# Kernel tuning notes

Measured on AMD Instinct MI355X. Metric: run time of the kernel, lower is better.

## Reference

```python
import jax, jax.numpy as jnp
from jax import lax
import numpy as np

B, C, H, W = 4, 256, 64, 64
CQK = C // 8  # 32


def conv3x3(x, w, b):
    # x: [B,C_in,H,W], w: [C_out,C_in,3,3], b: [C_out]
    y = lax.conv_general_dilated(x, w, window_strides=(1, 1), padding='SAME',
                                 dimension_numbers=('NCHW', 'OIHW', 'NCHW'))
    return y + b[None, :, None, None]


def setup_inputs() -> dict:
    key = jax.random.key(0)
    ks = jax.random.split(key, 8)
    scale = 0.02
    return {
        'x': jax.random.normal(ks[0], (B, C, H, W), dtype=jnp.float32),
        'wq': jax.random.normal(ks[1], (CQK, C, 3, 3), dtype=jnp.float32) * scale,
        'bq': jax.random.normal(ks[2], (CQK,), dtype=jnp.float32) * scale,
        'wk': jax.random.normal(ks[3], (CQK, C, 3, 3), dtype=jnp.float32) * scale,
        'bk': jax.random.normal(ks[4], (CQK,), dtype=jnp.float32) * scale,
        'wv': jax.random.normal(ks[5], (C, C, 3, 3), dtype=jnp.float32) * scale,
        'bv': jax.random.normal(ks[6], (C,), dtype=jnp.float32) * scale,
        'gamma': jax.random.normal(ks[7], (1,), dtype=jnp.float32) * scale,
    }


def reference(x, wq, bq, wk, bk, wv, bv, gamma):
    b, c, h, w = x.shape
    n = h * w
    # Q: [B, N, C//8]  (permute(0,2,1) of the flattened conv output)
    q = conv3x3(x, wq, bq).reshape(b, -1, n).transpose(0, 2, 1)
    # K: [B, C//8, N]
    k = conv3x3(x, wk, bk).reshape(b, -1, n)
    # s: [B, N_q, N_k]
    s = jnp.einsum('bqd,bdk->bqk', q, k)
    # NOTE: original uses Softmax(dim=-2), i.e. over the QUERY axis
    attn_T = jax.nn.softmax(s, axis=-2)
    # V: [B, C, N]
    v = conv3x3(x, wv, bv).reshape(b, c, n)
    # o = bmm(V, attn_T): [B, C, N]
    o = jnp.einsum('bcq,bqk->bck', v, attn_T).reshape(b, c, h, w)
    return x + gamma * o
```

## Files before the change

kernel.cpp:

```cpp
#include <hip/hip_runtime.h>
#include <cstddef>

#define N_PIX 4096
#define HW 64
#define LOG2E 1.4426950408889634f
#define SHIFT2 28.8539008177793f

typedef __attribute__((ext_vector_type(8))) short bf16x8;
typedef __attribute__((ext_vector_type(4))) float f32x4;

static __device__ __forceinline__ unsigned short f2bf(float f) {
    union { float f; unsigned u; } v; v.f = f;
    unsigned r = v.u + 0x7fffu + ((v.u >> 16) & 1u);
    return (unsigned short)(r >> 16);
}
static __device__ __forceinline__ float bf2f(unsigned short s) {
    union { unsigned u; float f; } v; v.u = (unsigned)s << 16;
    return v.f;
}
static __device__ __forceinline__ unsigned pack_bf16_trunc(float lo, float hi) {
    union { float f; unsigned u; } a, b; a.f = hi; b.f = lo;
    return __builtin_amdgcn_perm(a.u, b.u, 0x07060302u);
}

__global__ __launch_bounds__(256) void x_transpose(
    const float* __restrict__ x, unsigned short* __restrict__ xbf)
{
    __shared__ unsigned short Ts[64][72];
    const int tid = threadIdx.x;
    const int px0 = blockIdx.x * 64, ci0 = blockIdx.y * 64, b = blockIdx.z;
    const float* xb = x + ((size_t)b * 256 + ci0) * N_PIX;

#pragma unroll
    for (int r = 0; r < 4; ++r) {
        int c = r * 16 + (tid >> 4);
        int p4 = (tid & 15) * 4;
        float4 v = *(const float4*)&xb[(size_t)c * N_PIX + px0 + p4];
        Ts[c][p4 + 0] = f2bf(v.x);
        Ts[c][p4 + 1] = f2bf(v.y);
        Ts[c][p4 + 2] = f2bf(v.z);
        Ts[c][p4 + 3] = f2bf(v.w);
    }
    __syncthreads();
#pragma unroll
    for (int r = 0; r < 2; ++r) {
        int id = tid * 2 + r;
        int p = id >> 3, c8 = (id & 7) * 8;
        ushort4 lo, hi;
        lo.x = Ts[c8 + 0][p]; lo.y = Ts[c8 + 1][p];
        lo.z = Ts[c8 + 2][p]; lo.w = Ts[c8 + 3][p];
        hi.x = Ts[c8 + 4][p]; hi.y = Ts[c8 + 5][p];
        hi.z = Ts[c8 + 6][p]; hi.w = Ts[c8 + 7][p];
        size_t off = ((size_t)b * N_PIX + px0 + p) * 256 + ci0 + c8;
        *(ushort4*)&xbf[off]     = lo;
        *(ushort4*)&xbf[off + 4] = hi;
    }
}

__global__ __launch_bounds__(256) void w_transform(
    const float* __restrict__ wq, const float* __restrict__ wk,
    const float* __restrict__ wv, unsigned short* __restrict__ wAll)
{
    int gid = blockIdx.x * 256 + threadIdx.x;
    if (gid >= 72 * 320 * 4) return;
    int part = gid & 3;
    int m = (gid >> 2) % 320;
    int kb = gid / 1280;
    int t = kb >> 3;
    int ci0 = (kb & 7) * 32 + part * 8;
    const float* src; int co; float sc = 1.f;
    if (m < 256)      { src = wv; co = m; }
    else if (m < 288) { src = wq; co = m - 256; sc = LOG2E; }
    else              { src = wk; co = m - 288; }
    ushort4 lo, hi;
    lo.x = f2bf(sc * src[((size_t)co * 256 + ci0 + 0) * 9 + t]);
    lo.y = f2bf(sc * src[((size_t)co * 256 + ci0 + 1) * 9 + t]);
    lo.z = f2bf(sc * src[((size_t)co * 256 + ci0 + 2) * 9 + t]);
    lo.w = f2bf(sc * src[((size_t)co * 256 + ci0 + 3) * 9 + t]);
    hi.x = f2bf(sc * src[((size_t)co * 256 + ci0 + 4) * 9 + t]);
    hi.y = f2bf(sc * src[((size_t)co * 256 + ci0 + 5) * 9 + t]);
    hi.z = f2bf(sc * src[((size_t)co * 256 + ci0 + 6) * 9 + t]);
    hi.w = f2bf(sc * src[((size_t)co * 256 + ci0 + 7) * 9 + t]);
    size_t off = ((size_t)kb * 320 + m) * 32 + part * 8;
    *(ushort4*)&wAll[off]     = lo;
    *(ushort4*)&wAll[off + 4] = hi;
}

__global__ __launch_bounds__(256, 3) void conv_gemm_v3(
    const unsigned short* __restrict__ xbf, const unsigned short* __restrict__ wAll,
    const float* __restrict__ bq, const float* __restrict__ bk,
    const float* __restrict__ bv,
    unsigned short* __restrict__ vbf, unsigned short* __restrict__ qt,
    unsigned short* __restrict__ kt)
{
    const int tid = threadIdx.x;
    const int w = tid >> 6, lane = tid & 63, quad = lane >> 4, l15 = lane & 15;
    const int bx  = blockIdx.x;
    const int px0 = bx * 64;
    const int mt  = blockIdx.y;
    const int b   = blockIdx.z;
    const bool qk = (mt == 2);
    const int row0 = qk ? 256 : mt * 128;
    const int NCB  = qk ? 2 : 4;
    const int wc0  = (w & 1) * (qk ? 32 : 64);
    const int wp0  = (w >> 1) * 32;

    __shared__ unsigned short Bl[2][64 * 64];

    const unsigned short* xb = xbf + (size_t)b * N_PIX * 256;

    const int brow = tid >> 2;
    const int bp0  = (tid & 3) * 2;

    f32x4 acc[4][2];
#pragma unroll
    for (int cb = 0; cb < 4; ++cb)
#pragma unroll
        for (int jb = 0; jb < 2; ++jb) acc[cb][jb] = (f32x4){0.f, 0.f, 0.f, 0.f};

    const unsigned short* aBase = wAll + ((size_t)(row0 + wc0 + l15) * 32 + quad * 8);

    auto load_a = [&](int n, bf16x8 (&af)[2][4]) {
        const unsigned short* p = aBase + (size_t)(2 * n) * (320 * 32);
#pragma unroll
        for (int kl = 0; kl < 2; ++kl)
#pragma unroll
            for (int cb = 0; cb < 4; ++cb)
                if (cb < NCB) af[kl][cb] = *(const bf16x8*)&p[kl * (320 * 32) + cb * 512];
    };

    bf16x8 bS[2];
    auto load_b = [&](int n) {
        int t  = n >> 2;
        int ty = t / 3;
        int dy = ty - 1, dx = t - ty * 3 - 1;
        int gy = bx + dy, gx = brow + dx;
        int cio = (n & 3) * 64 + (tid & 3) * 16;
        if ((unsigned)gy < 64u && (unsigned)gx < 64u) {
            const unsigned short* s = xb + ((size_t)(gy * 64 + gx) * 256 + cio);
            bS[0] = *(const bf16x8*)&s[0];
            bS[1] = *(const bf16x8*)&s[8];
        } else {
            bS[0] = (bf16x8){0,0,0,0,0,0,0,0};
            bS[1] = (bf16x8){0,0,0,0,0,0,0,0};
        }
    };
    auto store_b = [&](int buf) {
        int p0 = (bp0 + brow) & 7;
        int p1 = (bp0 + 1 + brow) & 7;
        *(bf16x8*)&Bl[buf][brow * 64 + p0 * 8] = bS[0];
        *(bf16x8*)&Bl[buf][brow * 64 + p1 * 8] = bS[1];
    };

    auto step = [&](int n, bf16x8 (&cur)[2][4], bf16x8 (&nxt)[2][4]) {
        __syncthreads();
        const bool hasN = (n + 1 < 36);
        if (hasN) { load_b(n + 1); load_a(n + 1, nxt); }

        bf16x8 bf[2][2];
#pragma unroll
        for (int kl = 0; kl < 2; ++kl)
#pragma unroll
            for (int jb = 0; jb < 2; ++jb) {
                int row  = wp0 + jb * 16 + l15;
                int part = kl * 4 + quad;
                bf[kl][jb] = *(const bf16x8*)&Bl[n & 1][row * 64 + (((part + row) & 7) << 3)];
            }
#pragma unroll
        for (int kl = 0; kl < 2; ++kl)
#pragma unroll
            for (int cb = 0; cb < 4; ++cb)
                if (cb < NCB)
#pragma unroll
                    for (int jb = 0; jb < 2; ++jb)
                        acc[cb][jb] = __builtin_amdgcn_mfma_f32_16x16x32_bf16(
                            cur[kl][cb], bf[kl][jb], acc[cb][jb], 0, 0, 0);

        if (hasN) store_b((n + 1) & 1);
    };

    bf16x8 afA[2][4], afB[2][4];
    load_a(0, afA);
    load_b(0);
    store_b(0);

    for (int n = 0; n < 36; n += 2) {
        step(n,     afA, afB);
        step(n + 1, afB, afA);
    }

    if (!qk) {
#pragma unroll
        for (int cb = 0; cb < 4; ++cb) {
            int c = mt * 128 + wc0 + cb * 16 + quad * 4;
#pragma unroll
            for (int r = 0; r < 4; ++r) {
                float bias = bv[c + r];
#pragma unroll
                for (int jb = 0; jb < 2; ++jb) {
                    int px = px0 + wp0 + jb * 16 + l15;
                    vbf[((size_t)b * 256 + c + r) * N_PIX + px] = f2bf(acc[cb][jb][r] + bias);
                }
            }
        }
    } else {
#pragma unroll
        for (int cb = 0; cb < 2; ++cb) {
            int cl = wc0 + cb * 16 + quad * 4;
#pragma unroll
            for (int r = 0; r < 4; ++r) {
                int c = cl + r;
                float bias = (c < 32) ? bq[c] * LOG2E : bk[c - 32];
#pragma unroll
                for (int jb = 0; jb < 2; ++jb) {
                    int px = px0 + wp0 + jb * 16 + l15;
                    unsigned short val = f2bf(acc[cb][jb][r] + bias);
                    if (c < 32)
                        qt[((size_t)b * N_PIX + px) * 32 + c] = val;
                    else
                        kt[((size_t)b * N_PIX + px) * 32 + (c - 32)] = val;
                }
            }
        }
    }
}

__global__ __launch_bounds__(256, 2) void fused_attn_mfma(
    const unsigned short* __restrict__ qt, const unsigned short* __restrict__ kt,
    const unsigned short* __restrict__ vbf,
    unsigned short* __restrict__ Abuf, float* __restrict__ lbuf, int iRange)
{
    const int tid  = threadIdx.x;
    const int w    = tid >> 6;
    const int lane = tid & 63;
    const int quad = lane >> 4;
    const int l15  = lane & 15;
    const int j0   = blockIdx.x * 128;
    const int b    = blockIdx.y;
    const int sp   = blockIdx.z;
    const int iBeg = sp * iRange;
    const int NI   = iRange / 64;

    const unsigned short* qtb = qt + (size_t)b * N_PIX * 32;
    const unsigned short* ktb = kt + (size_t)b * N_PIX * 32;
    const unsigned short* vb  = vbf + (size_t)b * 256 * N_PIX;

    __shared__ unsigned Pfrag[2][4096];
    __shared__ float lred[4][128];

    bf16x8 kf[8];
#pragma unroll
    for (int jb = 0; jb < 8; ++jb)
        kf[jb] = *(const bf16x8*)&ktb[((size_t)(j0 + jb * 16 + l15)) * 32 + quad * 8];

    f32x4 acc[4][8];
#pragma unroll
    for (int cb = 0; cb < 4; ++cb)
#pragma unroll
        for (int jb = 0; jb < 8; ++jb)
            acc[cb][jb] = (f32x4){0.f, 0.f, 0.f, 0.f};

    float lpart[8] = {0.f, 0.f, 0.f, 0.f, 0.f, 0.f, 0.f, 0.f};

    const int wFrag = w >> 1;
    const int wL    = ((w & 1) << 5) + ((quad >> 1) << 4) + l15;
    const int wEl2  = (quad & 1) << 1;

    bf16x8 va[2][4];

    auto s_phase = [&](bf16x8 qa, int buf) {
#pragma unroll
        for (int jb = 0; jb < 8; ++jb) {
            f32x4 s = __builtin_amdgcn_mfma_f32_16x16x32_bf16(
                qa, kf[jb], (f32x4){-SHIFT2, -SHIFT2, -SHIFT2, -SHIFT2}, 0, 0, 0);
            float p0 = __builtin_amdgcn_exp2f(s[0]);
            float p1 = __builtin_amdgcn_exp2f(s[1]);
            float p2 = __builtin_amdgcn_exp2f(s[2]);
            float p3 = __builtin_amdgcn_exp2f(s[3]);
            lpart[jb] += (p0 + p1) + (p2 + p3);
            unsigned u0 = pack_bf16_trunc(p0, p1);
            unsigned u1 = pack_bf16_trunc(p2, p3);
            unsigned base = (((jb << 1) + wFrag) * 64 + wL) * 4 + wEl2;
            Pfrag[buf][base]     = u0;
            Pfrag[buf][base + 1] = u1;
        }
    };

    auto load_qa = [&](int i0) {
        return *(const bf16x8*)&qtb[((size_t)(i0 + w * 16 + l15)) * 32 + quad * 8];
    };
    auto load_va = [&](int i0) {
#pragma unroll
        for (int ks = 0; ks < 2; ++ks)
#pragma unroll
            for (int cb = 0; cb < 4; ++cb)
                va[ks][cb] = *(const bf16x8*)&vb[((size_t)(w * 64 + cb * 16 + l15)) * N_PIX
                                                 + i0 + ks * 32 + quad * 8];
    };

    load_va(iBeg);
    s_phase(load_qa(iBeg), 0);

    for (int n = 0; n < NI; ++n) {
        __syncthreads();
        const bool hasN = (n + 1 < NI);
        const int inext = iBeg + (n + 1) * 64;
        bf16x8 qaN;
        if (hasN) qaN = load_qa(inext);

#pragma unroll
        for (int ks = 0; ks < 2; ++ks) {
            bf16x8 pb[8];
#pragma unroll
            for (int jb = 0; jb < 8; ++jb)
                pb[jb] = *(const bf16x8*)&Pfrag[n & 1][(((jb << 1) + ks) * 64 + lane) * 4];
#pragma unroll
            for (int cb = 0; cb < 4; ++cb)
#pragma unroll
                for (int jb = 0; jb < 8; ++jb)
                    acc[cb][jb] = __builtin_amdgcn_mfma_f32_16x16x32_bf16(
                        va[ks][cb], pb[jb], acc[cb][jb], 0, 0, 0);
        }

        if (hasN) {
            load_va(inext);
            s_phase(qaN, (n + 1) & 1);
        }
    }

#pragma unroll
    for (int jb = 0; jb < 8; ++jb) {
        float v = lpart[jb];
        v += __shfl_xor(v, 16, 64);
        v += __shfl_xor(v, 32, 64);
        lpart[jb] = v;
    }
    if (lane < 16) {
#pragma unroll
        for (int jb = 0; jb < 8; ++jb)
            lred[w][jb * 16 + l15] = lpart[jb];
    }
    __syncthreads();
    if (tid < 128) {
        float s = lred[0][tid] + lred[1][tid] + lred[2][tid] + lred[3][tid];
        lbuf[((size_t)sp * 4 + b) * N_PIX + j0 + tid] = s;
    }

    unsigned short* Ab = Abuf + ((size_t)sp * 4 + b) * 256 * N_PIX;
#pragma unroll
    for (int cb = 0; cb < 4; ++cb) {
        int c = w * 64 + cb * 16 + quad * 4;
#pragma unroll
        for (int jb = 0; jb < 8; ++jb) {
            int j = j0 + jb * 16 + l15;
#pragma unroll
            for (int r = 0; r < 4; ++r)
                Ab[(size_t)(c + r) * N_PIX + j] = f2bf(acc[cb][jb][r]);
        }
    }
}

__global__ __launch_bounds__(256) void combine_kernel(
    const unsigned short* __restrict__ A, const float* __restrict__ L,
    const float* __restrict__ x, const float* __restrict__ gamma,
    float* __restrict__ out, int split)
{
    const size_t CH = (size_t)4 * 256 * N_PIX;
    size_t flat = ((size_t)blockIdx.x * 256 + threadIdx.x) * 8;
    int j = (int)(flat & (N_PIX - 1));
    int b = (int)(flat >> 20);

    float a[8] = {0.f, 0.f, 0.f, 0.f, 0.f, 0.f, 0.f, 0.f};
    float l[8] = {0.f, 0.f, 0.f, 0.f, 0.f, 0.f, 0.f, 0.f};
    for (int s = 0; s < split; ++s) {
        ushort4 av0 = *(const ushort4*)&A[flat + (size_t)s * CH];
        ushort4 av1 = *(const ushort4*)&A[flat + (size_t)s * CH + 4];
        a[0] += bf2f(av0.x); a[1] += bf2f(av0.y); a[2] += bf2f(av0.z); a[3] += bf2f(av0.w);
        a[4] += bf2f(av1.x); a[5] += bf2f(av1.y); a[6] += bf2f(av1.z); a[7] += bf2f(av1.w);
        float4 l0 = *(const float4*)&L[((size_t)s * 4 + b) * N_PIX + j];
        float4 l1 = *(const float4*)&L[((size_t)s * 4 + b) * N_PIX + j + 4];
        l[0] += l0.x; l[1] += l0.y; l[2] += l0.z; l[3] += l0.w;
        l[4] += l1.x; l[5] += l1.y; l[6] += l1.z; l[7] += l1.w;
    }
    float g = gamma[0];
    float4 x0 = *(const float4*)&x[flat];
    float4 x1 = *(const float4*)&x[flat + 4];
    float4 o0, o1;
    o0.x = x0.x + g * a[0] / l[0];
    o0.y = x0.y + g * a[1] / l[1];
    o0.z = x0.z + g * a[2] / l[2];
    o0.w = x0.w + g * a[3] / l[3];
    o1.x = x1.x + g * a[4] / l[4];
    o1.y = x1.y + g * a[5] / l[5];
    o1.z = x1.z + g * a[6] / l[6];
    o1.w = x1.w + g * a[7] / l[7];
    *(float4*)&out[flat]     = o0;
    *(float4*)&out[flat + 4] = o1;
}

extern "C" void kernel_launch(void* const* d_in, const int* in_sizes, int n_in,
                              void* d_out, int out_size, void* d_ws, size_t ws_size,
                              hipStream_t stream)
{
    const float* x     = (const float*)d_in[0];
    const float* wq    = (const float*)d_in[1];
    const float* bq    = (const float*)d_in[2];
    const float* wk    = (const float*)d_in[3];
    const float* bk    = (const float*)d_in[4];
    const float* wv    = (const float*)d_in[5];
    const float* bv    = (const float*)d_in[6];
    const float* gamma = (const float*)d_in[7];
    float* out = (float*)d_out;

    const size_t szQTel  = (size_t)4 * N_PIX * 32;
    const size_t szVBFel = (size_t)4 * 256 * N_PIX;
    const size_t szXBFel = (size_t)4 * N_PIX * 256;
    const size_t szWel   = (size_t)72 * 320 * 32;
    const size_t fixedB  = (2 * szQTel + szVBFel + szXBFel + szWel) * 2;

    int split = 4;
    while (split > 1) {
        size_t need = fixedB
                    + (size_t)split * 4 * 256 * N_PIX * 2
                    + (size_t)split * 4 * N_PIX * 4;
        if (need <= ws_size) break;
        split >>= 1;
    }

    unsigned short* Abuf = (unsigned short*)d_ws;
    float* lbuf = (float*)(Abuf + (size_t)split * 4 * 256 * N_PIX);
    unsigned short* qt   = (unsigned short*)(lbuf + (size_t)split * 4 * N_PIX);
    unsigned short* kt   = qt + szQTel;
    unsigned short* vbf  = kt + szQTel;
    unsigned short* xbf  = vbf + szVBFel;
    unsigned short* wAll = xbf + szXBFel;

    x_transpose<<<dim3(N_PIX / 64, 4, 4), 256, 0, stream>>>(x, xbf);
    w_transform<<<dim3((72 * 320 * 4 + 255) / 256), 256, 0, stream>>>(wq, wk, wv, wAll);

    conv_gemm_v3<<<dim3(N_PIX / 64, 3, 4), 256, 0, stream>>>(
        xbf, wAll, bq, bk, bv, vbf, qt, kt);

    fused_attn_mfma<<<dim3(N_PIX / 128, 4, split), 256, 0, stream>>>(
        qt, kt, vbf, Abuf, lbuf, N_PIX / split);

    combine_kernel<<<dim3((4 * 256 * N_PIX) / (256 * 8)), 256, 0, stream>>>(
        Abuf, lbuf, x, gamma, out, split);
}
```

Before: 188.4 us.

## Restructure conv GEMM to stage 3-row input halo in LDS once per block

Replaces the conv implicit-GEMM kernel with one where each 512-thread block handles one output image row and all 320 output channels (V, Q and K together). The block stages the three needed input rows, with zero-padded halo columns, into shared memory in two channel halves, and reuses them across all nine taps. This removes the per-tap reloading of input tiles from global memory and most of the per-step barriers. In exchange it uses about 53 KB of shared memory per block, more registers for 5x2 accumulators, and a smaller grid of 256 blocks, which may lower occupancy.

```diff
diff --git a/kernel.cpp b/kernel.cpp
--- a/kernel.cpp
+++ b/kernel.cpp
@@ -86,139 +86,168 @@
     *(ushort4*)&wAll[off + 4] = hi;
 }
 
-__global__ __launch_bounds__(256, 3) void conv_gemm_v3(
+__global__ __launch_bounds__(512, 2) void conv_gemm_v5(
     const unsigned short* __restrict__ xbf, const unsigned short* __restrict__ wAll,
     const float* __restrict__ bq, const float* __restrict__ bk,
     const float* __restrict__ bv,
     unsigned short* __restrict__ vbf, unsigned short* __restrict__ qt,
     unsigned short* __restrict__ kt)
 {
+    __shared__ unsigned short Xs[3 * 66 * 136];
+
     const int tid = threadIdx.x;
     const int w = tid >> 6, lane = tid & 63, quad = lane >> 4, l15 = lane & 15;
-    const int bx  = blockIdx.x;
-    const int px0 = bx * 64;
-    const int mt  = blockIdx.y;
-    const int b   = blockIdx.z;
-    const bool qk = (mt == 2);
-    const int row0 = qk ? 256 : mt * 128;
-    const int NCB  = qk ? 2 : 4;
-    const int wc0  = (w & 1) * (qk ? 32 : 64);
-    const int wp0  = (w >> 1) * 32;
-
-    __shared__ unsigned short Bl[2][64 * 64];
+    const int y = blockIdx.x;
+    const int b = blockIdx.y;
+    const int r0 = (w >> 1) * 80;
+    const int p0 = (w & 1) * 32;
 
     const unsigned short* xb = xbf + (size_t)b * N_PIX * 256;
-
-    const int brow = tid >> 2;
-    const int bp0  = (tid & 3) * 2;
-
-    f32x4 acc[4][2];
-#pragma unroll
-    for (int cb = 0; cb < 4; ++cb)
+    const unsigned short* aBase = wAll + ((size_t)(r0 + l15) * 32 + quad * 8);
+
+    const int scol = tid >> 3;
+    const int sg2  = (tid & 7) * 2;
+
+    bf16x8 S[3][2];
+    auto stage_load = [&](int h) {
+#pragma unroll
+        for (int ry = 0; ry < 3; ++ry) {
+            int gy = y + ry - 1;
+            if ((unsigned)gy < 64u) {
+                const unsigned short* s =
+                    xb + ((size_t)(gy * 64 + scol) * 256 + h * 128 + sg2 * 8);
+                S[ry][0] = *(const bf16x8*)&s[0];
+                S[ry][1] = *(const bf16x8*)&s[8];
+            } else {
+                S[ry][0] = (bf16x8){0,0,0,0,0,0,0,0};
+                S[ry][1] = (bf16x8){0,0,0,0,0,0,0,0};
+            }
+        }
+    };
+    auto stage_store = [&]() {
+#pragma unroll
+        for (int ry = 0; ry < 3; ++ry) {
+            *(bf16x8*)&Xs[(ry * 66 + scol + 1) * 136 + sg2 * 8]     = S[ry][0];
+            *(bf16x8*)&Xs[(ry * 66 + scol + 1) * 136 + sg2 * 8 + 8] = S[ry][1];
+        }
+    };
+
+    bf16x8 afA[2][5], afB[2][5];
+    auto load_a = [&](int kb, bf16x8 (&af)[2][5]) {
+        const unsigned short* p = aBase + (size_t)kb * 10240;
+#pragma unroll
+        for (int kl = 0; kl < 2; ++kl)
+#pragma unroll
+            for (int cb = 0; cb < 5; ++cb)
+                af[kl][cb] = *(const bf16x8*)&p[kl * 10240 + cb * 512];
+    };
+
+    bf16x8 bfA[2][2], bfB[2][2];
+    auto load_bf = [&](int t, int q2, bf16x8 (&bf)[2][2]) {
+        int ty = t / 3;
+        int dx = t - ty * 3 - 1;
+#pragma unroll
+        for (int kl = 0; kl < 2; ++kl)
+#pragma unroll
+            for (int jb = 0; jb < 2; ++jb) {
+                int sx = p0 + jb * 16 + l15 + dx + 1;
+                int cg = q2 * 8 + kl * 4 + quad;
+                bf[kl][jb] = *(const bf16x8*)&Xs[(ty * 66 + sx) * 136 + cg * 8];
+            }
+    };
+
+    f32x4 acc[5][2];
+#pragma unroll
+    for (int cb = 0; cb < 5; ++cb)
 #pragma unroll
         for (int jb = 0; jb < 2; ++jb) acc[cb][jb] = (f32x4){0.f, 0.f, 0.f, 0.f};
 
-    const unsigned short* aBase = wAll + ((size_t)(row0 + wc0 + l15) * 32 + quad * 8);
-
-    auto load_a = [&](int n, bf16x8 (&af)[2][4]) {
-        const unsigned short* p = aBase + (size_t)(2 * n) * (320 * 32);
+    auto mfma_step = [&](bf16x8 (&af)[2][5], bf16x8 (&bf)[2][2]) {
 #pragma unroll
         for (int kl = 0; kl < 2; ++kl)
 #pragma unroll
-            for (int cb = 0; cb < 4; ++cb)
-                if (cb < NCB) af[kl][cb] = *(const bf16x8*)&p[kl * (320 * 32) + cb * 512];
-    };
-
-    bf16x8 bS[2];
-    auto load_b = [&](int n) {
-        int t  = n >> 2;
-        int ty = t / 3;
-        int dy = ty - 1, dx = t - ty * 3 - 1;
-        int gy = bx + dy, gx = brow + dx;
-        int cio = (n & 3) * 64 + (tid & 3) * 16;
-        if ((unsigned)gy < 64u && (unsigned)gx < 64u) {
-            const unsigned short* s = xb + ((size_t)(gy * 64 + gx) * 256 + cio);
-            bS[0] = *(const bf16x8*)&s[0];
-            bS[1] = *(const bf16x8*)&s[8];
+            for (int cb = 0; cb < 5; ++cb)
+#pragma unroll
+                for (int jb = 0; jb < 2; ++jb)
+                    acc[cb][jb] = __builtin_amdgcn_mfma_f32_16x16x32_bf16(
+                        af[kl][cb], bf[kl][jb], acc[cb][jb], 0, 0, 0);
+    };
+
+    stage_load(0);
+    load_a(0, afA);
+    stage_store();
+    if (tid < 96) {
+        int ry = tid >> 5, rem = tid & 31;
+        int sx = (rem >> 4) ? 65 : 0;
+        int cg = rem & 15;
+        *(bf16x8*)&Xs[(ry * 66 + sx) * 136 + cg * 8] = (bf16x8){0,0,0,0,0,0,0,0};
+    }
+    __syncthreads();
+
+    stage_load(1);
+
+    load_bf(0, 0, bfA);
+#pragma unroll
+    for (int s = 0; s < 18; s += 2) {
+        const int t1 = (s + 1) >> 1, q1 = (s + 1) & 1;
+        load_a(t1 * 8 + q1 * 2, afB);
+        load_bf(t1, q1, bfB);
+        mfma_step(afA, bfA);
+        if (s + 2 < 18) {
+            const int t2 = (s + 2) >> 1, q2_ = (s + 2) & 1;
+            load_a(t2 * 8 + q2_ * 2, afA);
+            load_bf(t2, q2_, bfA);
         } else {
-            bS[0] = (bf16x8){0,0,0,0,0,0,0,0};
-            bS[1] = (bf16x8){0,0,0,0,0,0,0,0};
-        }
-    };
-    auto store_b = [&](int buf) {
-        int p0 = (bp0 + brow) & 7;
-        int p1 = (bp0 + 1 + brow) & 7;
-        *(bf16x8*)&Bl[buf][brow * 64 + p0 * 8] = bS[0];
-        *(bf16x8*)&Bl[buf][brow * 64 + p1 * 8] = bS[1];
-    };
-
-    auto step = [&](int n, bf16x8 (&cur)[2][4], bf16x8 (&nxt)[2][4]) {
-        __syncthreads();
-        const bool hasN = (n + 1 < 36);
-        if (hasN) { load_b(n + 1); load_a(n + 1, nxt); }
-
-        bf16x8 bf[2][2];
-#pragma unroll
-        for (int kl = 0; kl < 2; ++kl)
-#pragma unroll
-            for (int jb = 0; jb < 2; ++jb) {
-                int row  = wp0 + jb * 16 + l15;
-                int part = kl * 4 + quad;
-                bf[kl][jb] = *(const bf16x8*)&Bl[n & 1][row * 64 + (((part + row) & 7) << 3)];
-            }
-#pragma unroll
-        for (int kl = 0; kl < 2; ++kl)
-#pragma unroll
-            for (int cb = 0; cb < 4; ++cb)
-                if (cb < NCB)
-#pragma unroll
-                    for (int jb = 0; jb < 2; ++jb)
-                        acc[cb][jb] = __builtin_amdgcn_mfma_f32_16x16x32_bf16(
-                            cur[kl][cb], bf[kl][jb], acc[cb][jb], 0, 0, 0);
-
-        if (hasN) store_b((n + 1) & 1);
-    };
-
-    bf16x8 afA[2][4], afB[2][4];
-    load_a(0, afA);
-    load_b(0);
-    store_b(0);
-
-    for (int n = 0; n < 36; n += 2) {
-        step(n,     afA, afB);
-        step(n + 1, afB, afA);
-    }
-
-    if (!qk) {
-#pragma unroll
-        for (int cb = 0; cb < 4; ++cb) {
-            int c = mt * 128 + wc0 + cb * 16 + quad * 4;
-#pragma unroll
-            for (int r = 0; r < 4; ++r) {
-                float bias = bv[c + r];
+            load_a(4, afA);
+        }
+        mfma_step(afB, bfB);
+    }
+
+    __syncthreads();
+    stage_store();
+    __syncthreads();
+
+    load_bf(0, 0, bfA);
+#pragma unroll
+    for (int s = 0; s < 18; s += 2) {
+        const int t1 = (s + 1) >> 1, q1 = (s + 1) & 1;
+        load_a(t1 * 8 + 4 + q1 * 2, afB);
+        load_bf(t1, q1, bfB);
+        mfma_step(afA, bfA);
+        if (s + 2 < 18) {
+            const int t2 = (s + 2) >> 1, q2_ = (s + 2) & 1;
+            load_a(t2 * 8 + 4 + q2_ * 2, afA);
+            load_bf(t2, q2_, bfA);
+        }
+        mfma_step(afB, bfB);
+    }
+
+#pragma unroll
+    for (int cb = 0; cb < 5; ++cb) {
+        int cBase = r0 + cb * 16 + quad * 4;
+#pragma unroll
+        for (int r = 0; r < 4; ++r) {
+            int c = cBase + r;
+            if (c < 256) {
+                float bias = bv[c];
 #pragma unroll
                 for (int jb = 0; jb < 2; ++jb) {
-                    int px = px0 + wp0 + jb * 16 + l15;
-                    vbf[((size_t)b * 256 + c + r) * N_PIX + px] = f2bf(acc[cb][jb][r] + bias);
+                    int px = y * 64 + p0 + jb * 16 + l15;
+                    vbf[((size_t)b * 256 + c) * N_PIX + px] = f2bf(acc[cb][jb][r] + bias);
                 }
-            }
-        }
-    } else {
-#pragma unroll
-        for (int cb = 0; cb < 2; ++cb) {
-            int cl = wc0 + cb * 16 + quad * 4;
-#pragma unroll
-            for (int r = 0; r < 4; ++r) {
-                int c = cl + r;
-                float bias = (c < 32) ? bq[c] * LOG2E : bk[c - 32];
+            } else if (c < 288) {
+                float bias = bq[c - 256] * LOG2E;
 #pragma unroll
                 for (int jb = 0; jb < 2; ++jb) {
-                    int px = px0 + wp0 + jb * 16 + l15;
-                    unsigned short val = f2bf(acc[cb][jb][r] + bias);
-                    if (c < 32)
-                        qt[((size_t)b * N_PIX + px) * 32 + c] = val;
-                    else
-                        kt[((size_t)b * N_PIX + px) * 32 + (c - 32)] = val;
+                    int px = y * 64 + p0 + jb * 16 + l15;
+                    qt[((size_t)b * N_PIX + px) * 32 + (c - 256)] = f2bf(acc[cb][jb][r] + bias);
+                }
+            } else {
+                float bias = bk[c - 288];
+#pragma unroll
+                for (int jb = 0; jb < 2; ++jb) {
+                    int px = y * 64 + p0 + jb * 16 + l15;
+                    kt[((size_t)b * N_PIX + px) * 32 + (c - 288)] = f2bf(acc[cb][jb][r] + bias);
                 }
             }
         }
@@ -438,7 +467,7 @@
     x_transpose<<<dim3(N_PIX / 64, 4, 4), 256, 0, stream>>>(x, xbf);
     w_transform<<<dim3((72 * 320 * 4 + 255) / 256), 256, 0, stream>>>(wq, wk, wv, wAll);
 
-    conv_gemm_v3<<<dim3(N_PIX / 64, 3, 4), 256, 0, stream>>>(
+    conv_gemm_v5<<<dim3(HW, 4), 512, 0, stream>>>(
         xbf, wAll, bq, bk, bv, vbf, qt, kt);
 
     fused_attn_mfma<<<dim3(N_PIX / 128, 4, split), 256, 0, stream>>>(
```

Measured after the change: 197.3 us. +4.7%, slower.
